# Performance work log

Measured on AMD Instinct MI355X. Metric: run time of the kernel, lower is better.

Reference implementation:

```python
import jax, jax.numpy as jnp
import numpy as np

ITERS = 8
LAMBDA0 = 0.01
PAD = 1.0
LR = 1.0
EPS = 1e-12


def _sobel_grads(fmap):
    # kornia spatial_gradient: normalized 3x3 sobel (/8), replicate padding. fmap: C,H,W
    kx = jnp.array([[-1., 0., 1.], [-2., 0., 2.], [-1., 0., 1.]], fmap.dtype) / 8.0
    k = jnp.stack([kx, kx.T])[:, None]                       # 2,1,3,3 (OIHW)
    f = jnp.pad(fmap, ((0, 0), (1, 1), (1, 1)), mode='edge')[:, None]  # C,1,H+2,W+2
    g = jax.lax.conv_general_dilated(f, k, (1, 1), 'VALID')  # C,2,H,W
    return g[:, 0], g[:, 1]


def _bilinear(tensor, pts):
    # grid_sample bilinear, align_corners=True, at pixel coords. tensor: C,H,W; pts: N,2 (x,y) -> N,C
    c, h, w = tensor.shape
    x, y = pts[:, 0], pts[:, 1]
    x0 = jnp.clip(jnp.floor(x), 0, w - 1)
    y0 = jnp.clip(jnp.floor(y), 0, h - 1)
    x1 = jnp.clip(x0 + 1, 0, w - 1)
    y1 = jnp.clip(y0 + 1, 0, h - 1)
    wx, wy = x - x0, y - y0
    x0i, x1i = x0.astype(jnp.int32), x1.astype(jnp.int32)
    y0i, y1i = y0.astype(jnp.int32), y1.astype(jnp.int32)
    v00 = tensor[:, y0i, x0i]
    v01 = tensor[:, y0i, x1i]
    v10 = tensor[:, y1i, x0i]
    v11 = tensor[:, y1i, x1i]
    out = (v00 * (1 - wx) * (1 - wy) + v01 * wx * (1 - wy)
           + v10 * (1 - wx) * wy + v11 * wx * wy)
    return out.T


def _skew(v):
    x, y, z = v[..., 0], v[..., 1], v[..., 2]
    o = jnp.zeros_like(x)
    return jnp.stack([o, -z, y, z, o, -x, -y, x, o], -1).reshape(v.shape[:-1] + (3, 3))


def _so3exp(w):
    theta = jnp.linalg.norm(w)
    small = theta < 1e-7
    th = jnp.where(small, 1.0, theta)
    A = jnp.where(small, 1.0, jnp.sin(th) / th)
    B = jnp.where(small, 0.5, (1.0 - jnp.cos(th)) / th ** 2)
    W = _skew(w)
    return jnp.eye(3, dtype=w.dtype) + A * W + B * (W @ W)


def _normalize(x):
    return x / jnp.maximum(jnp.linalg.norm(x, axis=-1, keepdims=True), EPS)


def _pnp(p3D, feature_ref, feature_query, K, R_init, t_init):
    C, H, W = feature_query.shape
    gx, gy = _sobel_grads(feature_query)
    fref = _normalize(feature_ref)
    fx, fy, cx, cy = K[0, 0], K[1, 1], K[0, 2], K[1, 2]
    f_scale = jnp.stack([fx, fy])
    c_off = jnp.stack([cx, cy])

    def project(R, t):
        p3q = p3D @ R.T + t
        pn = p3q[:, :2] / p3q[:, 2:3]
        return p3q, pn, pn * f_scale + c_off

    def in_image(p2):
        return ((p2[:, 0] >= PAD) & (p2[:, 0] < W - PAD)
                & (p2[:, 1] >= PAD) & (p2[:, 1] < H - PAD))

    def masked_cost(p2, vf):
        f = _normalize(_bilinear(feature_query, p2))
        cost = ((f - fref) ** 2).sum(-1)
        return (cost * vf).sum() / vf.sum()

    R, t = R_init, t_init
    lam = jnp.asarray(LAMBDA0, p3D.dtype)
    jacobi = None
    cost_best = None
    p2D_init = None

    for i in range(ITERS):
        p3q, pn, p2 = project(R, t)
        if i == 0:
            p2D_init = jax.lax.stop_gradient(p2)
        vf = in_image(p2).astype(p3D.dtype)  # mask-weight == gather of valid pts

        f_raw = _bilinear(feature_query, p2)  # N,C
        norm = jnp.maximum(jnp.linalg.norm(f_raw, axis=-1, keepdims=True), EPS)
        f = f_raw / norm
        error = f - fref
        if i == 0:
            cost_best = (((error ** 2).sum(-1)) * vf).sum() / vf.sum()

        # Jacobian chain: J = J_f_p2 @ J_p2_pn @ J_pn_p3 @ J_p3_T   -> N,C,6
        x_, y_, d = p3q[:, 0], p3q[:, 1], p3q[:, 2]
        z = jnp.zeros_like(d)
        Jpn = jnp.stack([1 / d, z, -x_ / d ** 2,
                         z, 1 / d, -y_ / d ** 2], -1).reshape(-1, 2, 3)
        Jpn = Jpn * f_scale[None, :, None]  # fold in J_p2_pn = diag(fx,fy)
        Jp3T = jnp.concatenate(
            [jnp.broadcast_to(jnp.eye(3, dtype=p3D.dtype), p3q.shape[:-1] + (3, 3)),
             -_skew(p3q)], -1)  # N,3,6
        J26 = Jpn @ Jp3T       # N,2,6

        Jf = jnp.stack([_bilinear(gx, p2), _bilinear(gy, p2)], -1)  # N,C,2
        # normalize-feat Jacobian (I - f f^T)/||f_raw||, fused (no NxCxC)
        proj = jnp.einsum('nc,nck->nk', f, Jf)
        Jf = (Jf - f[:, :, None] * proj[:, None, :]) / norm[:, :, None]

        J = Jf @ J26  # N,C,6
        if i == 0:
            jacobi = 1.0 / (1.0 + jnp.linalg.norm(J * vf[:, None, None], axis=(0, 1)))
        J = J * jacobi

        Grad = jnp.einsum('ncj,nc,n->j', J, error, vf)
        Hess = jnp.einsum('nci,ncj,n->ij', J, J, vf)

        damp = jnp.diag(jnp.diagonal(Hess) + 1e-9) * lam  # LM damping
        delta = -LR * jnp.linalg.solve(Hess + damp, Grad)
        delta = delta * jacobi
        dt, dw = delta[:3], delta[3:6]
        dr = _so3exp(dw)
        R_new, t_new = dr @ R, dr @ t + dt

        _, _, p2_new = project(R_new, t_new)
        vf_new = in_image(p2_new).astype(p3D.dtype)
        cost_new = masked_cost(p2_new, vf_new)

        accept = cost_new <= cost_best
        lam = jnp.clip(lam * jnp.where(accept, 0.1, 10.0), 1e-8, 1e4)
        R = jnp.where(accept, R_new, R)
        t = jnp.where(accept, t_new, t)
        cost_best = jnp.where(accept, cost_new, cost_best)

    p3D_sg = jax.lax.stop_gradient(p3D)
    pf = p3D_sg @ R.T + t
    p2f = (pf[:, :2] / pf[:, 2:3]) * f_scale + c_off
    f_i = _normalize(_bilinear(feature_query, p2D_init))
    f_f = _normalize(_bilinear(feature_query, p2f))
    cost_init = ((fref - f_i) ** 2).sum(-1)
    cost_final = ((fref - f_f) ** 2).sum(-1)
    nan = jnp.asarray(jnp.nan, cost_init.dtype)
    cost_init = jnp.where(in_image(p2D_init), cost_init, nan)
    cost_final = jnp.where(in_image(p2f), cost_final, nan)
    return R, t, cost_init, cost_final


def setup_inputs() -> dict:
    N, C, H, W = 10000, 128, 512, 512
    key = jax.random.key(0)
    ks = jax.random.split(key, 4)
    xy = jax.random.uniform(ks[0], (N, 2), jnp.float32, -2.0, 2.0)
    z = jax.random.uniform(ks[1], (N, 1), jnp.float32, 4.0, 10.0)
    p3D = jnp.concatenate([xy, z], -1)
    feature_query = jax.random.normal(ks[2], (C, H, W), jnp.float32) * 0.5
    feature_ref = jax.random.normal(ks[3], (N, C), jnp.float32)
    K = jnp.array([[500., 0., 256.], [0., 500., 256.], [0., 0., 1.]], jnp.float32)
    R_init = _so3exp(jnp.array([0.01, -0.02, 0.015], jnp.float32))
    t_init = jnp.array([0.05, -0.03, 0.10], jnp.float32)
    return {"p3D": p3D, "feature_ref": feature_ref, "feature_query": feature_query,
            "K": K, "R_init": R_init, "t_init": t_init}


def reference(p3D, feature_ref, feature_query, K, R_init, t_init):
    return _pnp(p3D, feature_ref, feature_query, K, R_init, t_init)
```

## Files before the change

kernel.cpp:

```cpp
#include <hip/hip_runtime.h>
#include <hip/hip_fp16.h>
#include <math.h>

#define HW_ (512*512)

typedef float vf4 __attribute__((ext_vector_type(4)));

__device__ __forceinline__ float wred(float v){
#pragma unroll
  for (int o = 32; o > 0; o >>= 1) v += __shfl_xor(v, o, 64);
  return v;
}

template<bool TR>
__device__ __forceinline__ float2 tap(const void* __restrict__ f, int y, int x, int c0){
  if (TR){
    const __half2* p = (const __half2*)f + (((size_t)((y << 9) + x)) << 6) + (c0 >> 1);
    return __half22float2(*p);
  } else {
    const float* ff = (const float*)f;
    int base = (y << 9) + x;
    float2 r;
    r.x = ff[(size_t)c0 * HW_ + base];
    r.y = ff[(size_t)(c0 + 1) * HW_ + base];
    return r;
  }
}

__device__ __forceinline__ void fgrad(const float P[16], float w00, float w01, float w10, float w11,
                                      float& f, float& gx, float& gy){
  f = w00*P[5] + w01*P[6] + w10*P[9] + w11*P[10];
  float gx11 = (P[2]  + 2.f*P[6]  + P[10] - P[0] - 2.f*P[4]  - P[8] ) * 0.125f;
  float gx12 = (P[3]  + 2.f*P[7]  + P[11] - P[1] - 2.f*P[5]  - P[9] ) * 0.125f;
  float gx21 = (P[6]  + 2.f*P[10] + P[14] - P[4] - 2.f*P[8]  - P[12]) * 0.125f;
  float gx22 = (P[7]  + 2.f*P[11] + P[15] - P[5] - 2.f*P[9]  - P[13]) * 0.125f;
  gx = w00*gx11 + w01*gx12 + w10*gx21 + w11*gx22;
  float gy11 = (P[8]  + 2.f*P[9]  + P[10] - P[0] - 2.f*P[1]  - P[2] ) * 0.125f;
  float gy12 = (P[9]  + 2.f*P[10] + P[11] - P[1] - 2.f*P[2]  - P[3] ) * 0.125f;
  float gy21 = (P[12] + 2.f*P[13] + P[14] - P[4] - 2.f*P[5]  - P[6] ) * 0.125f;
  float gy22 = (P[13] + 2.f*P[14] + P[15] - P[5] - 2.f*P[6]  - P[7] ) * 0.125f;
  gy = w00*gy11 + w01*gy12 + w10*gy21 + w11*gy22;
}

template<bool TR>
__device__ __forceinline__ float cost_point(const void* __restrict__ fmap,
                                            const float* __restrict__ frn,
                                            int n, float px, float py, int lane){
  int c0 = 2 * lane;
  float x0f = fminf(fmaxf(floorf(px), 0.f), 511.f);
  float y0f = fminf(fmaxf(floorf(py), 0.f), 511.f);
  int x0 = (int)x0f, y0 = (int)y0f;
  int x1 = min(x0 + 1, 511), y1 = min(y0 + 1, 511);
  float wx = px - x0f, wy = py - y0f;
  float w00 = (1.f-wx)*(1.f-wy), w01 = wx*(1.f-wy), w10 = (1.f-wx)*wy, w11 = wx*wy;
  float2 a = tap<TR>(fmap, y0, x0, c0), b = tap<TR>(fmap, y0, x1, c0);
  float2 c = tap<TR>(fmap, y1, x0, c0), d = tap<TR>(fmap, y1, x1, c0);
  float f0 = w00*a.x + w01*b.x + w10*c.x + w11*d.x;
  float f1 = w00*a.y + w01*b.y + w10*c.y + w11*d.y;
  float nrm = fmaxf(sqrtf(wred(f0*f0 + f1*f1)), 1e-12f);
  const float2 fr = *(const float2*)(frn + (size_t)n*128 + c0);
  float e0 = f0/nrm - fr.x;
  float e1 = f1/nrm - fr.y;
  return wred(e0*e0 + e1*e1);
}

__global__ __launch_bounds__(256) void transpose_kernel(const float* __restrict__ fq,
                                                        __half* __restrict__ ftr){
  __shared__ float tf[256 * 32];
  int g  = blockIdx.x & 3;
  int sb = (blockIdx.x >> 2) << 8;
  int t = threadIdx.x;
  int l = t & 63, w = t >> 6;
  int s = l >> 4;
  int ipg = (l & 15) + (w << 4);
  int px0 = ipg << 2;
#pragma unroll
  for (int p = 0; p < 8; p++){
    int ch = s * 8 + p;
    const vf4* src = (const vf4*)(fq + (size_t)(g*32 + ch) * HW_ + sb + px0);
    vf4 v = __builtin_nontemporal_load(src);
#pragma unroll
    for (int j = 0; j < 4; j++){
      int px = px0 + j;
      int fz = ((3 * (px >> 2)) + ((px & 3) << 3)) & 31;
      tf[px * 32 + (ch ^ fz)] = v[j];
    }
  }
  __syncthreads();
#pragma unroll
  for (int q = 0; q < 4; q++){
    int px = (q << 6) + (t >> 2);
    int c8 = (t & 3) << 3;
    int fz = ((3 * (px >> 2)) + ((px & 3) << 3)) & 31;
    float v[8];
#pragma unroll
    for (int j = 0; j < 8; j++) v[j] = tf[px * 32 + ((c8 + j) ^ fz)];
    __half2 hh[4];
    hh[0] = __floats2half2_rn(v[0], v[1]);
    hh[1] = __floats2half2_rn(v[2], v[3]);
    hh[2] = __floats2half2_rn(v[4], v[5]);
    hh[3] = __floats2half2_rn(v[6], v[7]);
    *(uint4*)(ftr + ((size_t)(sb + px)) * 128 + g * 32 + c8) = *(uint4*)hh;
  }
}

__global__ __launch_bounds__(256) void prep_kernel(const float* __restrict__ fref,
                                                   float* __restrict__ frn,
                                                   const float* __restrict__ Rin,
                                                   const float* __restrict__ tin,
                                                   float* __restrict__ state, int N){
  if (blockIdx.x == 0){
    int t = threadIdx.x;
    if (t < 9) state[t] = Rin[t];
    if (t < 3) state[9 + t] = tin[t];
    if (t == 0) state[30] = 0.01f;
  }
  int lane = threadIdx.x & 63;
  int n = blockIdx.x * 4 + (threadIdx.x >> 6);
  if (n >= N) return;
  int c0 = 2 * lane;
  float2 fr = *(const float2*)(fref + (size_t)n*128 + c0);
  float rn = fmaxf(sqrtf(wred(fr.x*fr.x + fr.y*fr.y)), 1e-12f);
  float2 o; o.x = fr.x / rn; o.y = fr.y / rn;
  *(float2*)(frn + (size_t)n*128 + c0) = o;
}

template<bool TR>
__global__ __launch_bounds__(512) void eval_kernel(
    const float* __restrict__ p3D, const float* __restrict__ frn,
    const void* __restrict__ fmap, const float* __restrict__ Km,
    const float* __restrict__ state, int po, double* __restrict__ part, int N)
{
  int t = threadIdx.x;
  int lane = t & 63;
  int wv = t >> 6;
  int n = blockIdx.x * 8 + wv;
  double acc = 0.0;
  if (n < N){
    float fx = Km[0], fy = Km[4], cx = Km[2], cy = Km[5];
    float R0=state[po+0],R1=state[po+1],R2=state[po+2],R3=state[po+3],R4=state[po+4];
    float R5=state[po+5],R6=state[po+6],R7=state[po+7],R8=state[po+8];
    float t0=state[po+9], t1=state[po+10], t2=state[po+11];
    float PX = p3D[3*n], PY = p3D[3*n+1], PZ = p3D[3*n+2];
    float X = R0*PX + R1*PY + R2*PZ + t0;
    float Y = R3*PX + R4*PY + R5*PZ + t1;
    float D = R6*PX + R7*PY + R8*PZ + t2;
    float px = X / D * fx + cx;
    float py = Y / D * fy + cy;
    if (px >= 1.f && px < 511.f && py >= 1.f && py < 511.f){
      int c0 = 2 * lane;
      float x0f = fminf(fmaxf(floorf(px), 0.f), 511.f);
      float y0f = fminf(fmaxf(floorf(py), 0.f), 511.f);
      int x0 = (int)x0f, y0 = (int)y0f;
      int x1 = min(x0 + 1, 511), y1 = min(y0 + 1, 511);
      float wx = px - x0f, wy = py - y0f;
      int xs[4] = {max(x0-1,0), x0, x1, min(x1+1,511)};
      int ys[4] = {max(y0-1,0), y0, y1, min(y1+1,511)};
      float Pa[16], Pb[16];
#pragma unroll
      for (int r = 0; r < 4; r++)
#pragma unroll
        for (int scol = 0; scol < 4; scol++){
          float2 v = tap<TR>(fmap, ys[r], xs[scol], c0);
          Pa[r*4+scol] = v.x; Pb[r*4+scol] = v.y;
        }
      float w00 = (1.f-wx)*(1.f-wy), w01 = wx*(1.f-wy), w10 = (1.f-wx)*wy, w11 = wx*wy;
      float f0, gx0, gy0, f1, gx1, gy1;
      fgrad(Pa, w00, w01, w10, w11, f0, gx0, gy0);
      fgrad(Pb, w00, w01, w10, w11, f1, gx1, gy1);
      float nrm = fmaxf(sqrtf(wred(f0*f0 + f1*f1)), 1e-12f);
      float fc0 = f0 / nrm, fc1 = f1 / nrm;
      float projx = wred(fc0*gx0 + fc1*gx1);
      float projy = wred(fc0*gy0 + fc1*gy1);
      float jx0 = (gx0 - fc0*projx) / nrm, jx1 = (gx1 - fc1*projx) / nrm;
      float jy0 = (gy0 - fc0*projy) / nrm, jy1 = (gy1 - fc1*projy) / nrm;
      const float2 fr2 = *(const float2*)(frn + (size_t)n*128 + c0);
      float e0 = fc0 - fr2.x, e1 = fc1 - fr2.y;
      float se2 = wred(e0*e0 + e1*e1);
      float gex = wred(jx0*e0 + jx1*e1);
      float gey = wred(jy0*e0 + jy1*e1);
      float sxx = wred(jx0*jx0 + jx1*jx1);
      float sxy = wred(jx0*jy0 + jx1*jy1);
      float syy = wred(jy0*jy0 + jy1*jy1);
      float invD = 1.f / D;
      float rx = X * invD, ry = Y * invD;
      float A[6] = {fx*invD, 0.f, -fx*rx*invD, -fx*rx*ry, fx*(1.f+rx*rx), -fx*ry};
      float B[6] = {0.f, fy*invD, -fy*ry*invD, -fy*(1.f+ry*ry), fy*rx*ry, fy*rx};
      int li = 0, lj = 0;
      {
        const int pi_[21] = {0,0,0,0,0,0,1,1,1,1,1,2,2,2,2,3,3,3,4,4,5};
        const int pj_[21] = {0,1,2,3,4,5,1,2,3,4,5,2,3,4,5,3,4,5,4,5,5};
        if (lane >= 6 && lane < 27){ li = pi_[lane-6]; lj = pj_[lane-6]; }
      }
      float val = 0.f;
      if (lane < 6)        val = A[lane]*gex + B[lane]*gey;
      else if (lane < 27)  val = A[li]*A[lj]*sxx + (A[li]*B[lj] + A[lj]*B[li])*sxy + B[li]*B[lj]*syy;
      else if (lane == 27) val = se2;
      else if (lane == 28) val = 1.f;
      acc = (double)val;
    }
  }
  __shared__ double red[8][32];
  if (lane < 32) red[wv][lane] = acc;
  __syncthreads();
  if (t < 32){
    double s = 0.0;
#pragma unroll
    for (int i = 0; i < 8; i++) s += red[i][t];
    part[(size_t)blockIdx.x * 32 + t] = s;
  }
}

__device__ void solve_step(const double* __restrict__ cur, float* __restrict__ state){
  const int pi_[21] = {0,0,0,0,0,0,1,1,1,1,1,2,2,2,2,3,3,3,4,4,5};
  const int pj_[21] = {0,1,2,3,4,5,1,2,3,4,5,2,3,4,5,3,4,5,4,5,5};
  double rg[6]; for (int i = 0; i < 6; i++) rg[i] = cur[i];
  double rh[6][6];
  for (int k = 0; k < 21; k++){ rh[pi_[k]][pj_[k]] = cur[6+k]; rh[pj_[k]][pi_[k]] = cur[6+k]; }
  float jac[6];
  for (int j = 0; j < 6; j++) jac[j] = state[24+j];
  double lam = (double)state[30];
  double H[6][7];
  for (int i = 0; i < 6; i++)
    for (int j = 0; j < 6; j++) H[i][j] = (double)jac[i] * (double)jac[j] * rh[i][j];
  for (int i = 0; i < 6; i++) H[i][i] += (H[i][i] + 1e-9) * lam;
  for (int i = 0; i < 6; i++) H[i][6] = -((double)jac[i] * rg[i]);
  for (int k = 0; k < 6; k++){
    int p = k; double mx = fabs(H[k][k]);
    for (int r = k+1; r < 6; r++) if (fabs(H[r][k]) > mx){ mx = fabs(H[r][k]); p = r; }
    if (p != k) for (int c = k; c < 7; c++){ double tmp = H[k][c]; H[k][c] = H[p][c]; H[p][c] = tmp; }
    double inv = 1.0 / H[k][k];
    for (int r = k+1; r < 6; r++){
      double m = H[r][k] * inv;
      for (int c = k; c < 7; c++) H[r][c] -= m * H[k][c];
    }
  }
  double d[6];
  for (int i = 5; i >= 0; i--){
    double sx = H[i][6];
    for (int c = i+1; c < 6; c++) sx -= H[i][c] * d[c];
    d[i] = sx / H[i][i];
  }
  for (int j = 0; j < 6; j++) d[j] *= (double)jac[j];
  double wx = d[3], wy = d[4], wz = d[5];
  double th2 = wx*wx + wy*wy + wz*wz, th = sqrt(th2);
  double Aa, Bb;
  if (th < 1e-7){ Aa = 1.0; Bb = 0.5; } else { Aa = sin(th)/th; Bb = (1.0 - cos(th))/th2; }
  double W[3][3] = {{0,-wz,wy},{wz,0,-wx},{-wy,wx,0}};
  double W2[3][3];
  for (int i = 0; i < 3; i++) for (int j = 0; j < 3; j++){
    double q = 0; for (int k = 0; k < 3; k++) q += W[i][k]*W[k][j]; W2[i][j] = q;
  }
  double dr[3][3];
  for (int i = 0; i < 3; i++) for (int j = 0; j < 3; j++)
    dr[i][j] = (i == j ? 1.0 : 0.0) + Aa*W[i][j] + Bb*W2[i][j];
  double Rc[3][3], tc[3];
  for (int i = 0; i < 3; i++){ tc[i] = state[9+i]; for (int j = 0; j < 3; j++) Rc[i][j] = state[i*3+j]; }
  for (int i = 0; i < 3; i++){
    for (int j = 0; j < 3; j++){
      double q = 0; for (int k = 0; k < 3; k++) q += dr[i][k]*Rc[k][j];
      state[12 + i*3 + j] = (float)q;
    }
    double q = 0; for (int k = 0; k < 3; k++) q += dr[i][k]*tc[k];
    state[21 + i] = (float)(q + d[i]);
  }
}

__global__ __launch_bounds__(1024) void update_kernel(
    const double* __restrict__ part, int rows, float* __restrict__ state,
    double* __restrict__ cur, int iter)
{
  __shared__ double sm[32*32];
  __shared__ double tot[32];
  int t = threadIdx.x;
  int l = t & 31, ch = t >> 5;
  double s = 0.0;
  for (int r = ch; r < rows; r += 32) s += part[(size_t)r*32 + l];
  sm[ch*32 + l] = s;
  __syncthreads();
  if (t < 32){
    double x = 0.0;
    for (int c = 0; c < 32; c++) x += sm[c*32 + t];
    tot[t] = x;
  }
  __syncthreads();
  if (t != 0) return;

  if (iter < 0){
    const int diag_k[6] = {0, 6, 11, 15, 18, 20};
    for (int j = 0; j < 6; j++)
      state[24+j] = 1.0f / (1.0f + (float)sqrt(tot[6 + diag_k[j]]));
    state[31] = (float)(tot[27] / tot[28]);
    for (int k = 0; k < 32; k++) cur[k] = tot[k];
    solve_step(cur, state);
  } else {
    float cn = (float)(tot[27] / tot[28]);
    bool acpt = (cn <= state[31]);
    float lam = state[30] * (acpt ? 0.1f : 10.f);
    state[30] = fminf(fmaxf(lam, 1e-8f), 1e4f);
    if (acpt){
      for (int i = 0; i < 12; i++) state[i] = state[12+i];
      state[31] = cn;
      for (int k = 0; k < 32; k++) cur[k] = tot[k];
    }
    if (iter < 7) solve_step(cur, state);
  }
}

template<bool TR>
__global__ __launch_bounds__(256) void final_kernel(
    const float* __restrict__ p3D, const float* __restrict__ frn,
    const void* __restrict__ fmap, const float* __restrict__ Km,
    const float* __restrict__ Rin, const float* __restrict__ tin,
    const float* __restrict__ state, float* __restrict__ out, int N)
{
  if (blockIdx.x == 0 && threadIdx.x < 12) out[threadIdx.x] = state[threadIdx.x];
  int lane = threadIdx.x & 63;
  int n = blockIdx.x * 4 + (threadIdx.x >> 6);
  if (n >= N) return;
  float fx = Km[0], fy = Km[4], cx = Km[2], cy = Km[5];
  float PX = p3D[3*n], PY = p3D[3*n+1], PZ = p3D[3*n+2];
  const float nanv = __int_as_float(0x7fc00000);
  {
    float X = Rin[0]*PX + Rin[1]*PY + Rin[2]*PZ + tin[0];
    float Y = Rin[3]*PX + Rin[4]*PY + Rin[5]*PZ + tin[1];
    float D = Rin[6]*PX + Rin[7]*PY + Rin[8]*PZ + tin[2];
    float px = X / D * fx + cx, py = Y / D * fy + cy;
    bool vf = (px >= 1.f && px < 511.f && py >= 1.f && py < 511.f);
    float ci = nanv;
    if (vf) ci = cost_point<TR>(fmap, frn, n, px, py, lane);
    if (lane == 0) out[12 + n] = ci;
  }
  {
    float X = state[0]*PX + state[1]*PY + state[2]*PZ + state[9];
    float Y = state[3]*PX + state[4]*PY + state[5]*PZ + state[10];
    float D = state[6]*PX + state[7]*PY + state[8]*PZ + state[11];
    float px = X / D * fx + cx, py = Y / D * fy + cy;
    bool vf = (px >= 1.f && px < 511.f && py >= 1.f && py < 511.f);
    float cf = nanv;
    if (vf) cf = cost_point<TR>(fmap, frn, n, px, py, lane);
    if (lane == 0) out[12 + N + n] = cf;
  }
}

extern "C" void kernel_launch(void* const* d_in, const int* in_sizes, int n_in,
                              void* d_out, int out_size, void* d_ws, size_t ws_size,
                              hipStream_t stream)
{
  const float* p3D  = (const float*)d_in[0];
  const float* fref = (const float*)d_in[1];
  const float* fq   = (const float*)d_in[2];
  const float* Km   = (const float*)d_in[3];
  const float* Rin  = (const float*)d_in[4];
  const float* tin  = (const float*)d_in[5];
  float* out = (float*)d_out;
  int N = in_sizes[0] / 3;
  int NBLK  = (N + 7) / 8;
  int NBLK4 = (N + 3) / 4;

  char* w = (char*)d_ws;
  float*  state = (float*)w;
  double* cur   = (double*)(w + 256);
  size_t part_bytes = (size_t)NBLK * 32 * 8;
  double* part = (double*)(w + 512);
  float* frn = (float*)(w + 512 + part_bytes);
  size_t frn_bytes = (size_t)N * 128 * 4;
  size_t ftr_off = (512 + part_bytes + frn_bytes + 255) & ~(size_t)255;
  __half* ftr = (__half*)(w + ftr_off);
  size_t need = ftr_off + (size_t)HW_ * 128 * 2;
  bool tr = (ws_size >= need);

  if (tr) transpose_kernel<<<(HW_/256)*4, 256, 0, stream>>>(fq, ftr);
  const void* fmap = tr ? (const void*)ftr : (const void*)fq;
  prep_kernel<<<NBLK4, 256, 0, stream>>>(fref, frn, Rin, tin, state, N);

  if (tr) eval_kernel<true ><<<NBLK, 512, 0, stream>>>(p3D, frn, fmap, Km, state, 0, part, N);
  else    eval_kernel<false><<<NBLK, 512, 0, stream>>>(p3D, frn, fmap, Km, state, 0, part, N);
  update_kernel<<<1, 1024, 0, stream>>>(part, NBLK, state, cur, -1);

  for (int it = 0; it < 8; it++){
    if (tr) eval_kernel<true ><<<NBLK, 512, 0, stream>>>(p3D, frn, fmap, Km, state, 12, part, N);
    else    eval_kernel<false><<<NBLK, 512, 0, stream>>>(p3D, frn, fmap, Km, state, 12, part, N);
    update_kernel<<<1, 1024, 0, stream>>>(part, NBLK, state, cur, it);
  }
  if (tr) final_kernel<true ><<<NBLK4, 256, 0, stream>>>(p3D, frn, fmap, Km, Rin, tin, state, out, N);
  else    final_kernel<false><<<NBLK4, 256, 0, stream>>>(p3D, frn, fmap, Km, Rin, tin, state, out, N);
}
```

Baseline: 480.6 us.

## Restructure PnP pipeline: fuse normalisation, atomics reduction, cheaper final iteration

```diff
diff --git a/kernel.cpp b/kernel.cpp
--- a/kernel.cpp
+++ b/kernel.cpp
@@ -3,6 +3,7 @@
 #include <math.h>
 
 #define HW_ (512*512)
+#define CSTRIDE 32
 
 typedef float vf4 __attribute__((ext_vector_type(4)));
 
@@ -43,9 +44,9 @@
 }
 
 template<bool TR>
-__device__ __forceinline__ float cost_point(const void* __restrict__ fmap,
-                                            const float* __restrict__ frn,
-                                            int n, float px, float py, int lane){
+__device__ __forceinline__ float cost_point_raw(const void* __restrict__ fmap,
+                                                const float* __restrict__ fref,
+                                                int n, float px, float py, int lane){
   int c0 = 2 * lane;
   float x0f = fminf(fmaxf(floorf(px), 0.f), 511.f);
   float y0f = fminf(fmaxf(floorf(py), 0.f), 511.f);
@@ -57,157 +58,222 @@
   float2 c = tap<TR>(fmap, y1, x0, c0), d = tap<TR>(fmap, y1, x1, c0);
   float f0 = w00*a.x + w01*b.x + w10*c.x + w11*d.x;
   float f1 = w00*a.y + w01*b.y + w10*c.y + w11*d.y;
-  float nrm = fmaxf(sqrtf(wred(f0*f0 + f1*f1)), 1e-12f);
-  const float2 fr = *(const float2*)(frn + (size_t)n*128 + c0);
-  float e0 = f0/nrm - fr.x;
-  float e1 = f1/nrm - fr.y;
-  return wred(e0*e0 + e1*e1);
-}
-
-__global__ __launch_bounds__(256) void transpose_kernel(const float* __restrict__ fq,
-                                                        __half* __restrict__ ftr){
-  __shared__ float tf[256 * 32];
-  int g  = blockIdx.x & 3;
-  int sb = (blockIdx.x >> 2) << 8;
+  const float2 fr = *(const float2*)(fref + (size_t)n*128 + c0);
+  float Sff  = wred(f0*f0 + f1*f1);
+  float Sffr = wred(f0*fr.x + f1*fr.y);
+  float Sfr  = wred(fr.x*fr.x + fr.y*fr.y);
+  float inv = 1.f / fmaxf(sqrtf(Sff), 1e-12f);
+  float irn = 1.f / fmaxf(sqrtf(Sfr), 1e-12f);
+  return Sff*inv*inv - 2.f*Sffr*inv*irn + Sfr*irn*irn;
+}
+
+__global__ __launch_bounds__(512) void transpose_kernel(const float* __restrict__ fq,
+                                                        __half* __restrict__ ftr,
+                                                        double* __restrict__ cur2){
+  __shared__ __half tile[256 * 128];
   int t = threadIdx.x;
-  int l = t & 63, w = t >> 6;
-  int s = l >> 4;
-  int ipg = (l & 15) + (w << 4);
-  int px0 = ipg << 2;
-#pragma unroll
-  for (int p = 0; p < 8; p++){
-    int ch = s * 8 + p;
-    const vf4* src = (const vf4*)(fq + (size_t)(g*32 + ch) * HW_ + sb + px0);
-    vf4 v = __builtin_nontemporal_load(src);
+  if (blockIdx.x == 0 && t < 32) cur2[t * CSTRIDE] = 0.0;
+  int sb = blockIdx.x << 8;
+  int l = t & 63, r = t >> 6;
+  int px0 = l << 2;
+#pragma unroll
+  for (int p = 0; p < 16; p++){
+    int ch = p * 8 + r;
+    vf4 v = __builtin_nontemporal_load((const vf4*)(fq + (size_t)ch * HW_ + sb + px0));
 #pragma unroll
     for (int j = 0; j < 4; j++){
       int px = px0 + j;
-      int fz = ((3 * (px >> 2)) + ((px & 3) << 3)) & 31;
-      tf[px * 32 + (ch ^ fz)] = v[j];
+      tile[px * 128 + (ch ^ (px & 0x78))] = __float2half(v[j]);
     }
   }
   __syncthreads();
 #pragma unroll
-  for (int q = 0; q < 4; q++){
-    int px = (q << 6) + (t >> 2);
-    int c8 = (t & 3) << 3;
-    int fz = ((3 * (px >> 2)) + ((px & 3) << 3)) & 31;
-    float v[8];
-#pragma unroll
-    for (int j = 0; j < 8; j++) v[j] = tf[px * 32 + ((c8 + j) ^ fz)];
-    __half2 hh[4];
-    hh[0] = __floats2half2_rn(v[0], v[1]);
-    hh[1] = __floats2half2_rn(v[2], v[3]);
-    hh[2] = __floats2half2_rn(v[4], v[5]);
-    hh[3] = __floats2half2_rn(v[6], v[7]);
-    *(uint4*)(ftr + ((size_t)(sb + px)) * 128 + g * 32 + c8) = *(uint4*)hh;
-  }
-}
-
-__global__ __launch_bounds__(256) void prep_kernel(const float* __restrict__ fref,
-                                                   float* __restrict__ frn,
-                                                   const float* __restrict__ Rin,
-                                                   const float* __restrict__ tin,
-                                                   float* __restrict__ state, int N){
-  if (blockIdx.x == 0){
-    int t = threadIdx.x;
-    if (t < 9) state[t] = Rin[t];
-    if (t < 3) state[9 + t] = tin[t];
-    if (t == 0) state[30] = 0.01f;
-  }
-  int lane = threadIdx.x & 63;
-  int n = blockIdx.x * 4 + (threadIdx.x >> 6);
-  if (n >= N) return;
+  for (int p = 0; p < 8; p++){
+    int px = p * 32 + (t >> 4);
+    int c8 = (t & 15) << 3;
+    int cs = c8 ^ (px & 0x78);
+    uint4 v = *(const uint4*)&tile[px * 128 + cs];
+    *(uint4*)(ftr + ((size_t)(sb + px) << 7) + c8) = v;
+  }
+}
+
+__global__ void init_kernel(double* __restrict__ cur2){
+  if (threadIdx.x < 32) cur2[threadIdx.x * CSTRIDE] = 0.0;
+}
+
+template<bool TR>
+__device__ __forceinline__ bool gather_pt(
+    const float* __restrict__ p3D, const float* __restrict__ fref,
+    const void* __restrict__ fmap, const float* Rl, const float* Tl,
+    float fx, float fy, float cx, float cy,
+    int n, int lane, float s[10], float& X, float& Y, float& D)
+{
+  float PX = p3D[3*n], PY = p3D[3*n+1], PZ = p3D[3*n+2];
+  X = Rl[0]*PX + Rl[1]*PY + Rl[2]*PZ + Tl[0];
+  Y = Rl[3]*PX + Rl[4]*PY + Rl[5]*PZ + Tl[1];
+  D = Rl[6]*PX + Rl[7]*PY + Rl[8]*PZ + Tl[2];
+  float px = X / D * fx + cx;
+  float py = Y / D * fy + cy;
+  if (!(px >= 1.f && px < 511.f && py >= 1.f && py < 511.f)) return false;
   int c0 = 2 * lane;
-  float2 fr = *(const float2*)(fref + (size_t)n*128 + c0);
-  float rn = fmaxf(sqrtf(wred(fr.x*fr.x + fr.y*fr.y)), 1e-12f);
-  float2 o; o.x = fr.x / rn; o.y = fr.y / rn;
-  *(float2*)(frn + (size_t)n*128 + c0) = o;
+  float x0f = fminf(fmaxf(floorf(px), 0.f), 511.f);
+  float y0f = fminf(fmaxf(floorf(py), 0.f), 511.f);
+  int x0 = (int)x0f, y0 = (int)y0f;
+  int x1 = min(x0 + 1, 511), y1 = min(y0 + 1, 511);
+  float wx = px - x0f, wy = py - y0f;
+  int xs[4] = {max(x0-1,0), x0, x1, min(x1+1,511)};
+  int ys[4] = {max(y0-1,0), y0, y1, min(y1+1,511)};
+  float Pa[16], Pb[16];
+#pragma unroll
+  for (int rr = 0; rr < 4; rr++)
+#pragma unroll
+    for (int sc = 0; sc < 4; sc++){
+      float2 v = tap<TR>(fmap, ys[rr], xs[sc], c0);
+      Pa[rr*4+sc] = v.x; Pb[rr*4+sc] = v.y;
+    }
+  float w00 = (1.f-wx)*(1.f-wy), w01 = wx*(1.f-wy), w10 = (1.f-wx)*wy, w11 = wx*wy;
+  float f0, gx0, gy0, f1, gx1, gy1;
+  fgrad(Pa, w00, w01, w10, w11, f0, gx0, gy0);
+  fgrad(Pb, w00, w01, w10, w11, f1, gx1, gy1);
+  const float2 fr = *(const float2*)(fref + (size_t)n*128 + c0);
+  s[0] = f0*f0 + f1*f1;
+  s[1] = f0*fr.x + f1*fr.y;
+  s[2] = fr.x*fr.x + fr.y*fr.y;
+  s[3] = f0*gx0 + f1*gx1;
+  s[4] = f0*gy0 + f1*gy1;
+  s[5] = gx0*fr.x + gx1*fr.y;
+  s[6] = gy0*fr.x + gy1*fr.y;
+  s[7] = gx0*gx0 + gx1*gx1;
+  s[8] = gx0*gy0 + gx1*gy1;
+  s[9] = gy0*gy0 + gy1*gy1;
+  return true;
+}
+
+__device__ __forceinline__ float slot_val(const float s[10], float X, float Y, float D,
+                                          float fx, float fy, int lane, int li, int lj,
+                                          float& se2)
+{
+  float inv = 1.f / fmaxf(sqrtf(s[0]), 1e-12f);
+  float irn = 1.f / fmaxf(sqrtf(s[2]), 1e-12f);
+  float inv2 = inv*inv, inv3 = inv2*inv, inv4 = inv2*inv2;
+  float Sffr = s[1]*irn, Sgxfr = s[5]*irn, Sgyfr = s[6]*irn, Sfr = s[2]*irn*irn;
+  se2 = s[0]*inv2 - 2.f*Sffr*inv + Sfr;
+  float gex = s[3]*inv2 - Sgxfr*inv - s[3]*s[0]*inv4 + s[3]*Sffr*inv3;
+  float gey = s[4]*inv2 - Sgyfr*inv - s[4]*s[0]*inv4 + s[4]*Sffr*inv3;
+  float sxx = s[7]*inv2 - s[3]*s[3]*inv4;
+  float sxy = s[8]*inv2 - s[3]*s[4]*inv4;
+  float syy = s[9]*inv2 - s[4]*s[4]*inv4;
+  float invD = 1.f / D;
+  float rx = X * invD, ry = Y * invD;
+  float A[6] = {fx*invD, 0.f, -fx*rx*invD, -fx*rx*ry, fx*(1.f+rx*rx), -fx*ry};
+  float B[6] = {0.f, fy*invD, -fy*ry*invD, -fy*(1.f+ry*ry), fy*rx*ry, fy*rx};
+  float val = 0.f;
+  if (lane < 6)        val = A[lane]*gex + B[lane]*gey;
+  else if (lane < 27)  val = A[li]*A[lj]*sxx + (A[li]*B[lj] + A[lj]*B[li])*sxy + B[li]*B[lj]*syy;
+  else if (lane == 27) val = se2;
+  else if (lane == 28) val = 1.f;
+  return val;
 }
 
 template<bool TR>
 __global__ __launch_bounds__(512) void eval_kernel(
-    const float* __restrict__ p3D, const float* __restrict__ frn,
+    const float* __restrict__ p3D, const float* __restrict__ fref,
     const void* __restrict__ fmap, const float* __restrict__ Km,
-    const float* __restrict__ state, int po, double* __restrict__ part, int N)
+    const float* __restrict__ Rm, const float* __restrict__ tm,
+    double* __restrict__ cur2, float* __restrict__ cost_out, int N)
 {
   int t = threadIdx.x;
   int lane = t & 63;
   int wv = t >> 6;
-  int n = blockIdx.x * 8 + wv;
+  int gw = blockIdx.x * 8 + wv;
+  int n0 = gw * 2, n1 = n0 + 1;
+  float fx = Km[0], fy = Km[4], cx = Km[2], cy = Km[5];
+  float Rl[9], Tl[3];
+#pragma unroll
+  for (int i = 0; i < 9; i++) Rl[i] = Rm[i];
+#pragma unroll
+  for (int i = 0; i < 3; i++) Tl[i] = tm[i];
+  int li = 0, lj = 0;
+  {
+    const int pi_[21] = {0,0,0,0,0,0,1,1,1,1,1,2,2,2,2,3,3,3,4,4,5};
+    const int pj_[21] = {0,1,2,3,4,5,1,2,3,4,5,2,3,4,5,3,4,5,4,5,5};
+    if (lane >= 6 && lane < 27){ li = pi_[lane-6]; lj = pj_[lane-6]; }
+  }
+  float sA[10], sB[10];
+  float XA=0, YA=0, DA=1, XB=0, YB=0, DB=1;
+  bool vA = false, vB = false;
+  if (n0 < N) vA = gather_pt<TR>(p3D, fref, fmap, Rl, Tl, fx, fy, cx, cy, n0, lane, sA, XA, YA, DA);
+  if (n1 < N) vB = gather_pt<TR>(p3D, fref, fmap, Rl, Tl, fx, fy, cx, cy, n1, lane, sB, XB, YB, DB);
+  if (vA){
+#pragma unroll
+    for (int i = 0; i < 10; i++) sA[i] = wred(sA[i]);
+  }
+  if (vB){
+#pragma unroll
+    for (int i = 0; i < 10; i++) sB[i] = wred(sB[i]);
+  }
   double acc = 0.0;
-  if (n < N){
-    float fx = Km[0], fy = Km[4], cx = Km[2], cy = Km[5];
-    float R0=state[po+0],R1=state[po+1],R2=state[po+2],R3=state[po+3],R4=state[po+4];
-    float R5=state[po+5],R6=state[po+6],R7=state[po+7],R8=state[po+8];
-    float t0=state[po+9], t1=state[po+10], t2=state[po+11];
-    float PX = p3D[3*n], PY = p3D[3*n+1], PZ = p3D[3*n+2];
-    float X = R0*PX + R1*PY + R2*PZ + t0;
-    float Y = R3*PX + R4*PY + R5*PZ + t1;
-    float D = R6*PX + R7*PY + R8*PZ + t2;
-    float px = X / D * fx + cx;
-    float py = Y / D * fy + cy;
-    if (px >= 1.f && px < 511.f && py >= 1.f && py < 511.f){
-      int c0 = 2 * lane;
-      float x0f = fminf(fmaxf(floorf(px), 0.f), 511.f);
-      float y0f = fminf(fmaxf(floorf(py), 0.f), 511.f);
-      int x0 = (int)x0f, y0 = (int)y0f;
-      int x1 = min(x0 + 1, 511), y1 = min(y0 + 1, 511);
-      float wx = px - x0f, wy = py - y0f;
-      int xs[4] = {max(x0-1,0), x0, x1, min(x1+1,511)};
-      int ys[4] = {max(y0-1,0), y0, y1, min(y1+1,511)};
-      float Pa[16], Pb[16];
-#pragma unroll
-      for (int r = 0; r < 4; r++)
-#pragma unroll
-        for (int scol = 0; scol < 4; scol++){
-          float2 v = tap<TR>(fmap, ys[r], xs[scol], c0);
-          Pa[r*4+scol] = v.x; Pb[r*4+scol] = v.y;
-        }
-      float w00 = (1.f-wx)*(1.f-wy), w01 = wx*(1.f-wy), w10 = (1.f-wx)*wy, w11 = wx*wy;
-      float f0, gx0, gy0, f1, gx1, gy1;
-      fgrad(Pa, w00, w01, w10, w11, f0, gx0, gy0);
-      fgrad(Pb, w00, w01, w10, w11, f1, gx1, gy1);
-      float nrm = fmaxf(sqrtf(wred(f0*f0 + f1*f1)), 1e-12f);
-      float fc0 = f0 / nrm, fc1 = f1 / nrm;
-      float projx = wred(fc0*gx0 + fc1*gx1);
-      float projy = wred(fc0*gy0 + fc1*gy1);
-      float jx0 = (gx0 - fc0*projx) / nrm, jx1 = (gx1 - fc1*projx) / nrm;
-      float jy0 = (gy0 - fc0*projy) / nrm, jy1 = (gy1 - fc1*projy) / nrm;
-      const float2 fr2 = *(const float2*)(frn + (size_t)n*128 + c0);
-      float e0 = fc0 - fr2.x, e1 = fc1 - fr2.y;
-      float se2 = wred(e0*e0 + e1*e1);
-      float gex = wred(jx0*e0 + jx1*e1);
-      float gey = wred(jy0*e0 + jy1*e1);
-      float sxx = wred(jx0*jx0 + jx1*jx1);
-      float sxy = wred(jx0*jy0 + jx1*jy1);
-      float syy = wred(jy0*jy0 + jy1*jy1);
-      float invD = 1.f / D;
-      float rx = X * invD, ry = Y * invD;
-      float A[6] = {fx*invD, 0.f, -fx*rx*invD, -fx*rx*ry, fx*(1.f+rx*rx), -fx*ry};
-      float B[6] = {0.f, fy*invD, -fy*ry*invD, -fy*(1.f+ry*ry), fy*rx*ry, fy*rx};
-      int li = 0, lj = 0;
-      {
-        const int pi_[21] = {0,0,0,0,0,0,1,1,1,1,1,2,2,2,2,3,3,3,4,4,5};
-        const int pj_[21] = {0,1,2,3,4,5,1,2,3,4,5,2,3,4,5,3,4,5,4,5,5};
-        if (lane >= 6 && lane < 27){ li = pi_[lane-6]; lj = pj_[lane-6]; }
-      }
-      float val = 0.f;
-      if (lane < 6)        val = A[lane]*gex + B[lane]*gey;
-      else if (lane < 27)  val = A[li]*A[lj]*sxx + (A[li]*B[lj] + A[lj]*B[li])*sxy + B[li]*B[lj]*syy;
-      else if (lane == 27) val = se2;
-      else if (lane == 28) val = 1.f;
-      acc = (double)val;
-    }
+  float se2A = 0.f, se2B = 0.f;
+  if (vA) acc += (double)slot_val(sA, XA, YA, DA, fx, fy, lane, li, lj, se2A);
+  if (vB) acc += (double)slot_val(sB, XB, YB, DB, fx, fy, lane, li, lj, se2B);
+  if (cost_out && lane == 0){
+    const float nanv = __int_as_float(0x7fc00000);
+    if (n0 < N) cost_out[n0] = vA ? se2A : nanv;
+    if (n1 < N) cost_out[n1] = vB ? se2B : nanv;
   }
   __shared__ double red[8][32];
   if (lane < 32) red[wv][lane] = acc;
   __syncthreads();
   if (t < 32){
-    double s = 0.0;
-#pragma unroll
-    for (int i = 0; i < 8; i++) s += red[i][t];
-    part[(size_t)blockIdx.x * 32 + t] = s;
+    double ssum = 0.0;
+#pragma unroll
+    for (int i = 0; i < 8; i++) ssum += red[i][t];
+    if (ssum != 0.0) atomicAdd(&cur2[t * CSTRIDE], ssum);
+  }
+}
+
+template<bool TR>
+__global__ __launch_bounds__(512) void cost_kernel(
+    const float* __restrict__ p3D, const float* __restrict__ fref,
+    const void* __restrict__ fmap, const float* __restrict__ Km,
+    const float* __restrict__ Rm, const float* __restrict__ tm,
+    double* __restrict__ cur2, int N)
+{
+  int t = threadIdx.x;
+  int lane = t & 63;
+  int wv = t >> 6;
+  int gw = blockIdx.x * 8 + wv;
+  int n0 = gw * 2, n1 = n0 + 1;
+  float fx = Km[0], fy = Km[4], cx = Km[2], cy = Km[5];
+  float Rl[9], Tl[3];
+#pragma unroll
+  for (int i = 0; i < 9; i++) Rl[i] = Rm[i];
+#pragma unroll
+  for (int i = 0; i < 3; i++) Tl[i] = tm[i];
+  double accc = 0.0, accn = 0.0;
+#pragma unroll
+  for (int q = 0; q < 2; q++){
+    int n = q ? n1 : n0;
+    if (n >= N) continue;
+    float PX = p3D[3*n], PY = p3D[3*n+1], PZ = p3D[3*n+2];
+    float X = Rl[0]*PX + Rl[1]*PY + Rl[2]*PZ + Tl[0];
+    float Y = Rl[3]*PX + Rl[4]*PY + Rl[5]*PZ + Tl[1];
+    float D = Rl[6]*PX + Rl[7]*PY + Rl[8]*PZ + Tl[2];
+    float px = X / D * fx + cx, py = Y / D * fy + cy;
+    if (px >= 1.f && px < 511.f && py >= 1.f && py < 511.f){
+      float cp = cost_point_raw<TR>(fmap, fref, n, px, py, lane);
+      accc += (double)cp; accn += 1.0;
+    }
+  }
+  double acc = (lane == 27) ? accc : ((lane == 28) ? accn : 0.0);
+  __shared__ double red[8][32];
+  if (lane < 32) red[wv][lane] = acc;
+  __syncthreads();
+  if (t < 32){
+    double ssum = 0.0;
+#pragma unroll
+    for (int i = 0; i < 8; i++) ssum += red[i][t];
+    if (ssum != 0.0) atomicAdd(&cur2[t * CSTRIDE], ssum);
   }
 }
 
@@ -266,27 +332,18 @@
   }
 }
 
-__global__ __launch_bounds__(1024) void update_kernel(
-    const double* __restrict__ part, int rows, float* __restrict__ state,
-    double* __restrict__ cur, int iter)
-{
-  __shared__ double sm[32*32];
-  __shared__ double tot[32];
-  int t = threadIdx.x;
-  int l = t & 31, ch = t >> 5;
-  double s = 0.0;
-  for (int r = ch; r < rows; r += 32) s += part[(size_t)r*32 + l];
-  sm[ch*32 + l] = s;
-  __syncthreads();
-  if (t < 32){
-    double x = 0.0;
-    for (int c = 0; c < 32; c++) x += sm[c*32 + t];
-    tot[t] = x;
-  }
-  __syncthreads();
-  if (t != 0) return;
-
+__global__ void update_kernel(double* __restrict__ cur2, float* __restrict__ state,
+                              double* __restrict__ cur,
+                              const float* __restrict__ Rin, const float* __restrict__ tin,
+                              int iter)
+{
+  if (threadIdx.x != 0) return;
+  double tot[32];
+  for (int i = 0; i < 32; i++){ tot[i] = cur2[i * CSTRIDE]; cur2[i * CSTRIDE] = 0.0; }
   if (iter < 0){
+    for (int i = 0; i < 9; i++) state[i] = Rin[i];
+    for (int i = 0; i < 3; i++) state[9+i] = tin[i];
+    state[30] = 0.01f;
     const int diag_k[6] = {0, 6, 11, 15, 18, 20};
     for (int j = 0; j < 6; j++)
       state[24+j] = 1.0f / (1.0f + (float)sqrt(tot[6 + diag_k[j]]));
@@ -309,9 +366,8 @@
 
 template<bool TR>
 __global__ __launch_bounds__(256) void final_kernel(
-    const float* __restrict__ p3D, const float* __restrict__ frn,
+    const float* __restrict__ p3D, const float* __restrict__ fref,
     const void* __restrict__ fmap, const float* __restrict__ Km,
-    const float* __restrict__ Rin, const float* __restrict__ tin,
     const float* __restrict__ state, float* __restrict__ out, int N)
 {
   if (blockIdx.x == 0 && threadIdx.x < 12) out[threadIdx.x] = state[threadIdx.x];
@@ -320,27 +376,14 @@
   if (n >= N) return;
   float fx = Km[0], fy = Km[4], cx = Km[2], cy = Km[5];
   float PX = p3D[3*n], PY = p3D[3*n+1], PZ = p3D[3*n+2];
-  const float nanv = __int_as_float(0x7fc00000);
-  {
-    float X = Rin[0]*PX + Rin[1]*PY + Rin[2]*PZ + tin[0];
-    float Y = Rin[3]*PX + Rin[4]*PY + Rin[5]*PZ + tin[1];
-    float D = Rin[6]*PX + Rin[7]*PY + Rin[8]*PZ + tin[2];
-    float px = X / D * fx + cx, py = Y / D * fy + cy;
-    bool vf = (px >= 1.f && px < 511.f && py >= 1.f && py < 511.f);
-    float ci = nanv;
-    if (vf) ci = cost_point<TR>(fmap, frn, n, px, py, lane);
-    if (lane == 0) out[12 + n] = ci;
-  }
-  {
-    float X = state[0]*PX + state[1]*PY + state[2]*PZ + state[9];
-    float Y = state[3]*PX + state[4]*PY + state[5]*PZ + state[10];
-    float D = state[6]*PX + state[7]*PY + state[8]*PZ + state[11];
-    float px = X / D * fx + cx, py = Y / D * fy + cy;
-    bool vf = (px >= 1.f && px < 511.f && py >= 1.f && py < 511.f);
-    float cf = nanv;
-    if (vf) cf = cost_point<TR>(fmap, frn, n, px, py, lane);
-    if (lane == 0) out[12 + N + n] = cf;
-  }
+  float X = state[0]*PX + state[1]*PY + state[2]*PZ + state[9];
+  float Y = state[3]*PX + state[4]*PY + state[5]*PZ + state[10];
+  float D = state[6]*PX + state[7]*PY + state[8]*PZ + state[11];
+  float px = X / D * fx + cx, py = Y / D * fy + cy;
+  bool vf = (px >= 1.f && px < 511.f && py >= 1.f && py < 511.f);
+  float cf = __int_as_float(0x7fc00000);
+  if (vf) cf = cost_point_raw<TR>(fmap, fref, n, px, py, lane);
+  if (lane == 0) out[12 + N + n] = cf;
 }
 
 extern "C" void kernel_launch(void* const* d_in, const int* in_sizes, int n_in,
@@ -355,34 +398,35 @@
   const float* tin  = (const float*)d_in[5];
   float* out = (float*)d_out;
   int N = in_sizes[0] / 3;
-  int NBLK  = (N + 7) / 8;
+  int NEB   = (N + 15) / 16;
   int NBLK4 = (N + 3) / 4;
 
   char* w = (char*)d_ws;
   float*  state = (float*)w;
   double* cur   = (double*)(w + 256);
-  size_t part_bytes = (size_t)NBLK * 32 * 8;
-  double* part = (double*)(w + 512);
-  float* frn = (float*)(w + 512 + part_bytes);
-  size_t frn_bytes = (size_t)N * 128 * 4;
-  size_t ftr_off = (512 + part_bytes + frn_bytes + 255) & ~(size_t)255;
+  double* cur2  = (double*)(w + 512);
+  size_t ftr_off = (512 + 32 * CSTRIDE * 8 + 255) & ~(size_t)255;
   __half* ftr = (__half*)(w + ftr_off);
   size_t need = ftr_off + (size_t)HW_ * 128 * 2;
   bool tr = (ws_size >= need);
 
-  if (tr) transpose_kernel<<<(HW_/256)*4, 256, 0, stream>>>(fq, ftr);
+  if (tr) transpose_kernel<<<HW_/256, 512, 0, stream>>>(fq, ftr, cur2);
+  else    init_kernel<<<1, 64, 0, stream>>>(cur2);
   const void* fmap = tr ? (const void*)ftr : (const void*)fq;
-  prep_kernel<<<NBLK4, 256, 0, stream>>>(fref, frn, Rin, tin, state, N);
-
-  if (tr) eval_kernel<true ><<<NBLK, 512, 0, stream>>>(p3D, frn, fmap, Km, state, 0, part, N);
-  else    eval_kernel<false><<<NBLK, 512, 0, stream>>>(p3D, frn, fmap, Km, state, 0, part, N);
-  update_kernel<<<1, 1024, 0, stream>>>(part, NBLK, state, cur, -1);
-
-  for (int it = 0; it < 8; it++){
-    if (tr) eval_kernel<true ><<<NBLK, 512, 0, stream>>>(p3D, frn, fmap, Km, state, 12, part, N);
-    else    eval_kernel<false><<<NBLK, 512, 0, stream>>>(p3D, frn, fmap, Km, state, 12, part, N);
-    update_kernel<<<1, 1024, 0, stream>>>(part, NBLK, state, cur, it);
-  }
-  if (tr) final_kernel<true ><<<NBLK4, 256, 0, stream>>>(p3D, frn, fmap, Km, Rin, tin, state, out, N);
-  else    final_kernel<false><<<NBLK4, 256, 0, stream>>>(p3D, frn, fmap, Km, Rin, tin, state, out, N);
-}
+
+  if (tr) eval_kernel<true ><<<NEB, 512, 0, stream>>>(p3D, fref, fmap, Km, Rin, tin, cur2, out + 12, N);
+  else    eval_kernel<false><<<NEB, 512, 0, stream>>>(p3D, fref, fmap, Km, Rin, tin, cur2, out + 12, N);
+  update_kernel<<<1, 64, 0, stream>>>(cur2, state, cur, Rin, tin, -1);
+
+  for (int it = 0; it < 7; it++){
+    if (tr) eval_kernel<true ><<<NEB, 512, 0, stream>>>(p3D, fref, fmap, Km, state + 12, state + 21, cur2, nullptr, N);
+    else    eval_kernel<false><<<NEB, 512, 0, stream>>>(p3D, fref, fmap, Km, state + 12, state + 21, cur2, nullptr, N);
+    update_kernel<<<1, 64, 0, stream>>>(cur2, state, cur, Rin, tin, it);
+  }
+  if (tr) cost_kernel<true ><<<NEB, 512, 0, stream>>>(p3D, fref, fmap, Km, state + 12, state + 21, cur2, N);
+  else    cost_kernel<false><<<NEB, 512, 0, stream>>>(p3D, fref, fmap, Km, state + 12, state + 21, cur2, N);
+  update_kernel<<<1, 64, 0, stream>>>(cur2, state, cur, Rin, tin, 7);
+
+  if (tr) final_kernel<true ><<<NBLK4, 256, 0, stream>>>(p3D, fref, fmap, Km, state, out, N);
+  else    final_kernel<false><<<NBLK4, 256, 0, stream>>>(p3D, fref, fmap, Km, state, out, N);
+}
```

New measurement: 485.5 us. About the same (+1.0%).
